# Kernel optimization log

Hardware: AMD Instinct MI355X
Metric: run time of the kernel (lower is better)

Reference implementation:

```python
import jax, jax.numpy as jnp
import numpy as np
import math

H = 8  # num_heads

def setup_inputs() -> dict:
    key = jax.random.key(0)
    ks = jax.random.split(key, 12)
    B, N, M, k = 2, 8192, 8192, 32
    dq, dk, dv = 256, 256, 256
    s = 1.0 / math.sqrt(dq)
    inp = {
        'Q': jax.random.normal(ks[0], (B, N, dq), dtype=jnp.float32),
        'K': jax.random.normal(ks[1], (B, M, dk), dtype=jnp.float32),
        'neighbours': jax.random.randint(ks[2], (B, N, k), 0, M),
        'Wq': jax.random.normal(ks[3], (dq, dv), dtype=jnp.float32) * s,
        'bq': jnp.zeros((dv,), dtype=jnp.float32),
        'Wk': jax.random.normal(ks[4], (dk, dv), dtype=jnp.float32) * s,
        'bk': jnp.zeros((dv,), dtype=jnp.float32),
        'Wv': jax.random.normal(ks[5], (dk, dv), dtype=jnp.float32) * s,
        'bv': jnp.zeros((dv,), dtype=jnp.float32),
        'Wo': jax.random.normal(ks[6], (dv, dv), dtype=jnp.float32) * (1.0 / math.sqrt(dv)),
        'bo': jnp.zeros((dv,), dtype=jnp.float32),
    }
    return inp

def reference(Q, K, neighbours, Wq, bq, Wk, bk, Wv, bv, Wo, bo):
    B, N, _ = Q.shape
    dv = Wq.shape[1]
    ds = dv // H
    # project and split heads (contiguous channel chunks == reshape)
    Qh = (Q @ Wq + bq).reshape(B, N, H, ds)            # [B,N,H,ds]
    Kh = (K @ Wk + bk).reshape(B, -1, H, ds)           # [B,M,H,ds]
    Vh = (K @ Wv + bv).reshape(B, -1, H, ds)           # [B,M,H,ds]
    # gather per-node kNN neighbour keys/values: [B,N,k,H,ds]
    gather = jax.vmap(lambda x, idx: x[idx])
    Kn = gather(Kh, neighbours)
    Vn = gather(Vh, neighbours)
    # scale uses full latent size (faithful to original), not head dim
    scale = 1.0 / math.sqrt(dv)
    E = jnp.einsum('bnhd,bnkhd->bnhk', Qh, Kn) * scale  # [B,N,H,k]
    A = jax.nn.softmax(E, axis=-1)
    AV = jnp.einsum('bnhk,bnkhd->bnhd', A, Vn).reshape(B, N, dv)
    return AV @ Wo + bo
```

## Files before the change

kernel.cpp:

```cpp
#include <hip/hip_runtime.h>
#include <hip/hip_bf16.h>
#include <stdint.h>

typedef unsigned short u16;
typedef __attribute__((ext_vector_type(8))) short short8;
typedef __attribute__((ext_vector_type(4))) float f32x4;

__device__ __forceinline__ u16 f2bf(float f) {
    union { float f; unsigned int i; } v; v.f = f;
    unsigned int b = v.i;
    return (u16)((b + 0x7FFFu + ((b >> 16) & 1u)) >> 16);
}

__device__ __forceinline__ short8 cvt8(float4 a, float4 b) {
    union { __hip_bfloat162 h[4]; short8 s; } u;
    u.h[0] = __float22bfloat162_rn(make_float2(a.x, a.y));
    u.h[1] = __float22bfloat162_rn(make_float2(a.z, a.w));
    u.h[2] = __float22bfloat162_rn(make_float2(b.x, b.y));
    u.h[3] = __float22bfloat162_rn(make_float2(b.z, b.w));
    return u.s;
}

typedef const __attribute__((address_space(1))) void* as1cv;
typedef __attribute__((address_space(3))) void* as3v;
__device__ __forceinline__ void gload16(const void* g, void* l) {
    __builtin_amdgcn_global_load_lds((as1cv)g, (as3v)l, 16, 0, 0);
}

__global__ __launch_bounds__(256) void wprep(
    const float* __restrict__ W0, const float* __restrict__ W1,
    const float* __restrict__ W2, const float* __restrict__ W3,
    u16* __restrict__ T0, u16* __restrict__ T1,
    u16* __restrict__ T2, u16* __restrict__ T3)
{
    const float* W = blockIdx.z == 0 ? W0 : blockIdx.z == 1 ? W1 : blockIdx.z == 2 ? W2 : W3;
    u16*        T  = blockIdx.z == 0 ? T0 : blockIdx.z == 1 ? T1 : blockIdx.z == 2 ? T2 : T3;
    __shared__ u16 ts[64][65];
    int k0 = blockIdx.x * 64, n0 = blockIdx.y * 64;
    int t = threadIdx.x;
    int r = t >> 2, cq = (t & 3) * 16;
    const float4* src = reinterpret_cast<const float4*>(W + (k0 + r) * 256 + n0 + cq);
    for (int u = 0; u < 4; ++u) {
        float4 v = src[u];
        int c = cq + u * 4;
        ts[r][c + 0] = f2bf(v.x); ts[r][c + 1] = f2bf(v.y);
        ts[r][c + 2] = f2bf(v.z); ts[r][c + 3] = f2bf(v.w);
    }
    __syncthreads();
    u16* dst = T + (n0 + r) * 256 + k0 + cq;
    for (int u = 0; u < 16; ++u) dst[u] = ts[cq + u][r];
}

__global__ __launch_bounds__(256) void gemm_proj(
    const float* __restrict__ Q, const float* __restrict__ K,
    const u16* __restrict__ Wtq, const u16* __restrict__ Wtk, const u16* __restrict__ Wtv,
    const float* __restrict__ bq, const float* __restrict__ bk, const float* __restrict__ bv,
    u16* __restrict__ Qh, u16* __restrict__ Kh, u16* __restrict__ Vh)
{
    int z = blockIdx.z;
    const float* Af   = (z == 0) ? Q   : K;
    const u16*   Wt   = (z == 0) ? Wtq : (z == 1) ? Wtk : Wtv;
    const float* bias = (z == 0) ? bq  : (z == 1) ? bk  : bv;
    u16*         C    = (z == 0) ? Qh  : (z == 1) ? Kh  : Vh;

    __shared__ float Asf[128 * 64];
    __shared__ u16   Bs[128 * 64];

    int t = threadIdx.x;
    int lane = t & 63, w = t >> 6;
    int row0 = blockIdx.x * 128, col0 = blockIdx.y * 128;
    int wr = (w >> 1) * 64, wc = (w & 1) * 64;
    int qd = lane >> 4, md = lane & 15;

    f32x4 acc[4][4] = {};

    for (int kt = 0; kt < 256; kt += 64) {
#pragma unroll
        for (int u = 0; u < 8; ++u) {
            int chunk = w * 8 + u;
            int s = chunk * 64 + lane;
            int r = s >> 4, c = s & 15;
            gload16(Af + (size_t)(row0 + r) * 256 + kt + ((c ^ (r & 15)) * 4),
                    (char*)Asf + chunk * 1024);
        }
#pragma unroll
        for (int u = 0; u < 4; ++u) {
            int chunk = w * 4 + u;
            int s = chunk * 64 + lane;
            int r = s >> 3, c = s & 7;
            gload16(Wt + (size_t)(col0 + r) * 256 + kt + ((c ^ (r & 7)) * 8),
                    (char*)Bs + chunk * 1024);
        }
        __syncthreads();
#pragma unroll
        for (int ks = 0; ks < 64; ks += 32) {
            short8 af[4], bf[4];
#pragma unroll
            for (int i = 0; i < 4; ++i) {
                int ar = wr + i * 16 + md;
                int c0 = (ks >> 2) + qd * 2;
                int x = ar & 15;
                float4 fa0 = reinterpret_cast<const float4*>(Asf)[ar * 16 + (c0 ^ x)];
                float4 fa1 = reinterpret_cast<const float4*>(Asf)[ar * 16 + ((c0 + 1) ^ x)];
                af[i] = cvt8(fa0, fa1);
            }
#pragma unroll
            for (int j = 0; j < 4; ++j) {
                int br = wc + j * 16 + md;
                int slot = ((ks >> 3) + qd) ^ (br & 7);
                bf[j] = reinterpret_cast<const short8*>(Bs)[br * 8 + slot];
            }
#pragma unroll
            for (int i = 0; i < 4; ++i)
#pragma unroll
                for (int j = 0; j < 4; ++j)
                    acc[i][j] = __builtin_amdgcn_mfma_f32_16x16x32_bf16(
                        af[i], bf[j], acc[i][j], 0, 0, 0);
        }
        __syncthreads();
    }

#pragma unroll
    for (int i = 0; i < 4; ++i)
#pragma unroll
        for (int j = 0; j < 4; ++j) {
            int col = col0 + wc + j * 16 + md;
            float b = bias[col];
#pragma unroll
            for (int r = 0; r < 4; ++r) {
                int row = row0 + wr + i * 16 + qd * 4 + r;
                C[(size_t)row * 256 + col] = f2bf(acc[i][j][r] + b);
            }
        }
}

__global__ __launch_bounds__(256) void gemm_out(
    const u16* __restrict__ Ab, const u16* __restrict__ Wt,
    const float* __restrict__ bias, float* __restrict__ Cout)
{
    __shared__ u16 As[64 * 64];
    __shared__ u16 Bs[128 * 64];

    int t = threadIdx.x;
    int lane = t & 63, w = t >> 6;
    int row0 = blockIdx.x * 64, col0 = blockIdx.y * 128;
    int wr = (w >> 1) * 32, wc = (w & 1) * 64;
    int qd = lane >> 4, md = lane & 15;

    f32x4 acc[2][4] = {};

    for (int kt = 0; kt < 256; kt += 64) {
#pragma unroll
        for (int u = 0; u < 2; ++u) {
            int chunk = w * 2 + u;
            int s = chunk * 64 + lane;
            int r = s >> 3, c = s & 7;
            gload16(Ab + (size_t)(row0 + r) * 256 + kt + ((c ^ (r & 7)) * 8),
                    (char*)As + chunk * 1024);
        }
#pragma unroll
        for (int u = 0; u < 4; ++u) {
            int chunk = w * 4 + u;
            int s = chunk * 64 + lane;
            int r = s >> 3, c = s & 7;
            gload16(Wt + (size_t)(col0 + r) * 256 + kt + ((c ^ (r & 7)) * 8),
                    (char*)Bs + chunk * 1024);
        }
        __syncthreads();
#pragma unroll
        for (int ks = 0; ks < 64; ks += 32) {
            short8 af[2], bf[4];
#pragma unroll
            for (int i = 0; i < 2; ++i) {
                int ar = wr + i * 16 + md;
                int slot = ((ks >> 3) + qd) ^ (ar & 7);
                af[i] = reinterpret_cast<const short8*>(As)[ar * 8 + slot];
            }
#pragma unroll
            for (int j = 0; j < 4; ++j) {
                int br = wc + j * 16 + md;
                int slot = ((ks >> 3) + qd) ^ (br & 7);
                bf[j] = reinterpret_cast<const short8*>(Bs)[br * 8 + slot];
            }
#pragma unroll
            for (int i = 0; i < 2; ++i)
#pragma unroll
                for (int j = 0; j < 4; ++j)
                    acc[i][j] = __builtin_amdgcn_mfma_f32_16x16x32_bf16(
                        af[i], bf[j], acc[i][j], 0, 0, 0);
        }
        __syncthreads();
    }

#pragma unroll
    for (int i = 0; i < 2; ++i)
#pragma unroll
        for (int j = 0; j < 4; ++j) {
            int col = col0 + wc + j * 16 + md;
            float b = bias[col];
#pragma unroll
            for (int r = 0; r < 4; ++r) {
                int row = row0 + wr + i * 16 + qd * 4 + r;
                Cout[(size_t)row * 256 + col] = acc[i][j][r] + b;
            }
        }
}

__global__ __launch_bounds__(256) void attn(
    const u16* __restrict__ Qh, const u16* __restrict__ Kh, const u16* __restrict__ Vh,
    const int* __restrict__ nbr, u16* __restrict__ AVb)
{
    __shared__ float qs[4][256];
    __shared__ float as_[4][256];
    __shared__ int jb[4][32];

    int t = threadIdx.x;
    int row0 = blockIdx.x * 4;
    int b = row0 >> 13;

#pragma unroll
    for (int rr = 0; rr < 2; ++rr) {
        int idx = rr * 256 + t;
        int r = idx >> 7, c = (idx & 127) * 2;
        unsigned int v = *reinterpret_cast<const unsigned int*>(
            Qh + (size_t)(row0 + r) * 256 + c);
        union { unsigned int i; float f; } lo, hi;
        lo.i = v << 16; hi.i = v & 0xffff0000u;
        qs[r][c] = lo.f; qs[r][c + 1] = hi.f;
    }
    if (t < 128) {
        int r = t >> 5, j = t & 31;
        int ji = nbr[(size_t)(row0 + r) * 32 + j];
        jb[r][j] = ((b << 13) + ji) << 9;
    }
    __syncthreads();

    int h = t >> 5, j = t & 31;
#pragma unroll
    for (int r = 0; r < 4; ++r) {
        const char* kp = (const char*)Kh + jb[r][j] + h * 64;
        uint4 kw[4];
        kw[0] = *reinterpret_cast<const uint4*>(kp);
        kw[1] = *reinterpret_cast<const uint4*>(kp + 16);
        kw[2] = *reinterpret_cast<const uint4*>(kp + 32);
        kw[3] = *reinterpret_cast<const uint4*>(kp + 48);
        const float* q = &qs[r][h * 32];
        float e = 0.f;
#pragma unroll
        for (int cq4 = 0; cq4 < 4; ++cq4) {
            unsigned int wds[4] = {kw[cq4].x, kw[cq4].y, kw[cq4].z, kw[cq4].w};
#pragma unroll
            for (int u = 0; u < 4; ++u) {
                union { unsigned int i; float f; } lo, hi;
                lo.i = wds[u] << 16; hi.i = wds[u] & 0xffff0000u;
                e += q[cq4 * 8 + u * 2] * lo.f + q[cq4 * 8 + u * 2 + 1] * hi.f;
            }
        }
        e *= 0.0625f;
        float m = e;
        for (int off = 16; off; off >>= 1) m = fmaxf(m, __shfl_xor(m, off, 32));
        float p = __expf(e - m);
        float s = p;
        for (int off = 16; off; off >>= 1) s += __shfl_xor(s, off, 32);
        as_[r][t] = p / s;
    }
    __syncthreads();

    {
        int r = t >> 6, c2 = t & 63;
        int hh = c2 >> 3;
        float wv[32];
#pragma unroll
        for (int u = 0; u < 8; ++u)
            *reinterpret_cast<float4*>(&wv[u * 4]) =
                *reinterpret_cast<const float4*>(&as_[r][hh * 32 + u * 4]);
        float a0 = 0.f, a1 = 0.f, a2 = 0.f, a3 = 0.f;
#pragma unroll
        for (int jj = 0; jj < 32; ++jj) {
            int off = __builtin_amdgcn_readfirstlane(jb[r][jj]);
            uint2 v = *reinterpret_cast<const uint2*>(
                (const char*)Vh + off + c2 * 8);
            union { unsigned int i; float f; } l0, h0, l1, h1;
            l0.i = v.x << 16; h0.i = v.x & 0xffff0000u;
            l1.i = v.y << 16; h1.i = v.y & 0xffff0000u;
            float wgt = wv[jj];
            a0 += wgt * l0.f; a1 += wgt * h0.f;
            a2 += wgt * l1.f; a3 += wgt * h1.f;
        }
        u16 o[4] = {f2bf(a0), f2bf(a1), f2bf(a2), f2bf(a3)};
        *reinterpret_cast<uint2*>(AVb + (size_t)(row0 + r) * 256 + c2 * 4) =
            *reinterpret_cast<const uint2*>(o);
    }
}

extern "C" void kernel_launch(void* const* d_in, const int* in_sizes, int n_in,
                              void* d_out, int out_size, void* d_ws, size_t ws_size,
                              hipStream_t stream) {
    const float* Q   = (const float*)d_in[0];
    const float* K   = (const float*)d_in[1];
    const int*   nbr = (const int*)d_in[2];
    const float* Wq  = (const float*)d_in[3];
    const float* bq  = (const float*)d_in[4];
    const float* Wk  = (const float*)d_in[5];
    const float* bk  = (const float*)d_in[6];
    const float* Wv  = (const float*)d_in[7];
    const float* bv  = (const float*)d_in[8];
    const float* Wo  = (const float*)d_in[9];
    const float* bo  = (const float*)d_in[10];
    float* out = (float*)d_out;

    char* ws = (char*)d_ws;
    size_t off = 0;
    auto alloc = [&](size_t bytes) -> void* {
        void* p = ws + off;
        off += (bytes + 255) & ~(size_t)255;
        return p;
    };
    const size_t MN = 16384;
    u16* Wtq = (u16*)alloc(256 * 256 * 2);
    u16* Wtk = (u16*)alloc(256 * 256 * 2);
    u16* Wtv = (u16*)alloc(256 * 256 * 2);
    u16* Wto = (u16*)alloc(256 * 256 * 2);
    u16* Qh  = (u16*)alloc(MN * 256 * 2);
    u16* Kh  = (u16*)alloc(MN * 256 * 2);
    u16* Vh  = (u16*)alloc(MN * 256 * 2);
    u16* AVb = (u16*)alloc(MN * 256 * 2);

    wprep<<<dim3(4, 4, 4), 256, 0, stream>>>(Wq, Wk, Wv, Wo, Wtq, Wtk, Wtv, Wto);
    gemm_proj<<<dim3(128, 2, 3), 256, 0, stream>>>(Q, K, Wtq, Wtk, Wtv,
                                                   bq, bk, bv, Qh, Kh, Vh);
    attn<<<dim3(4096), 256, 0, stream>>>(Qh, Kh, Vh, nbr, AVb);
    gemm_out<<<dim3(256, 2), 256, 0, stream>>>(AVb, Wto, bo, out);
}
```

Measured before the change: 171.0 us.

## Restructure kNN attention kernel to one wave per row with register softmax

The attention kernel now assigns one 64-lane wave per query row. Each half-wave handles 16 neighbours, and each lane covers 8 contiguous channels loaded as 16-byte vectors. Q stays in registers, the scores are reduced with lane shuffles, and the softmax is computed in registers before the V accumulation. This removes the shared-memory staging of Q and the attention weights and one of the block barriers, and it widens the V loads. In exchange it adds more shuffles and register pressure, and it drops the explicit __syncthreads after jbs is written. That is safe only because each wave reads only its own jbs row, which relies on wave-synchronous execution.

```diff
diff --git a/kernel.cpp b/kernel.cpp
--- a/kernel.cpp
+++ b/kernel.cpp
@@ -25,6 +25,12 @@
 typedef __attribute__((address_space(3))) void* as3v;
 __device__ __forceinline__ void gload16(const void* g, void* l) {
     __builtin_amdgcn_global_load_lds((as1cv)g, (as3v)l, 16, 0, 0);
+}
+
+__device__ __forceinline__ void up2(unsigned int v, float& lo, float& hi) {
+    union { unsigned int i; float f; } a, b;
+    a.i = v << 16; b.i = v & 0xffff0000u;
+    lo = a.f; hi = b.f;
 }
 
 __global__ __launch_bounds__(256) void wprep(
@@ -210,86 +216,79 @@
     const u16* __restrict__ Qh, const u16* __restrict__ Kh, const u16* __restrict__ Vh,
     const int* __restrict__ nbr, u16* __restrict__ AVb)
 {
-    __shared__ float qs[4][256];
-    __shared__ float as_[4][256];
-    __shared__ int jb[4][32];
+    __shared__ int jbs[4][32];
 
     int t = threadIdx.x;
-    int row0 = blockIdx.x * 4;
-    int b = row0 >> 13;
-
-#pragma unroll
-    for (int rr = 0; rr < 2; ++rr) {
-        int idx = rr * 256 + t;
-        int r = idx >> 7, c = (idx & 127) * 2;
-        unsigned int v = *reinterpret_cast<const unsigned int*>(
-            Qh + (size_t)(row0 + r) * 256 + c);
-        union { unsigned int i; float f; } lo, hi;
-        lo.i = v << 16; hi.i = v & 0xffff0000u;
-        qs[r][c] = lo.f; qs[r][c + 1] = hi.f;
-    }
-    if (t < 128) {
-        int r = t >> 5, j = t & 31;
-        int ji = nbr[(size_t)(row0 + r) * 32 + j];
-        jb[r][j] = ((b << 13) + ji) << 9;
-    }
-    __syncthreads();
-
-    int h = t >> 5, j = t & 31;
-#pragma unroll
-    for (int r = 0; r < 4; ++r) {
-        const char* kp = (const char*)Kh + jb[r][j] + h * 64;
-        uint4 kw[4];
-        kw[0] = *reinterpret_cast<const uint4*>(kp);
-        kw[1] = *reinterpret_cast<const uint4*>(kp + 16);
-        kw[2] = *reinterpret_cast<const uint4*>(kp + 32);
-        kw[3] = *reinterpret_cast<const uint4*>(kp + 48);
-        const float* q = &qs[r][h * 32];
-        float e = 0.f;
-#pragma unroll
-        for (int cq4 = 0; cq4 < 4; ++cq4) {
-            unsigned int wds[4] = {kw[cq4].x, kw[cq4].y, kw[cq4].z, kw[cq4].w};
-#pragma unroll
-            for (int u = 0; u < 4; ++u) {
-                union { unsigned int i; float f; } lo, hi;
-                lo.i = wds[u] << 16; hi.i = wds[u] & 0xffff0000u;
-                e += q[cq4 * 8 + u * 2] * lo.f + q[cq4 * 8 + u * 2 + 1] * hi.f;
-            }
-        }
-        e *= 0.0625f;
-        float m = e;
-        for (int off = 16; off; off >>= 1) m = fmaxf(m, __shfl_xor(m, off, 32));
-        float p = __expf(e - m);
-        float s = p;
-        for (int off = 16; off; off >>= 1) s += __shfl_xor(s, off, 32);
-        as_[r][t] = p / s;
-    }
-    __syncthreads();
-
+    int w = t >> 6, lane = t & 63;
+    int row = blockIdx.x * 4 + w;
+    int b = row >> 13;
+    int bbase = b << 13;
+
+    int c8 = lane & 31;
+    int jh = lane >> 5;
+
+    if (lane < 32) {
+        int ji = nbr[(size_t)row * 32 + lane];
+        jbs[w][lane] = (bbase + ji) * 256;
+    }
+
+    float qf[8];
     {
-        int r = t >> 6, c2 = t & 63;
-        int hh = c2 >> 3;
-        float wv[32];
-#pragma unroll
-        for (int u = 0; u < 8; ++u)
-            *reinterpret_cast<float4*>(&wv[u * 4]) =
-                *reinterpret_cast<const float4*>(&as_[r][hh * 32 + u * 4]);
-        float a0 = 0.f, a1 = 0.f, a2 = 0.f, a3 = 0.f;
-#pragma unroll
-        for (int jj = 0; jj < 32; ++jj) {
-            int off = __builtin_amdgcn_readfirstlane(jb[r][jj]);
-            uint2 v = *reinterpret_cast<const uint2*>(
-                (const char*)Vh + off + c2 * 8);
-            union { unsigned int i; float f; } l0, h0, l1, h1;
-            l0.i = v.x << 16; h0.i = v.x & 0xffff0000u;
-            l1.i = v.y << 16; h1.i = v.y & 0xffff0000u;
-            float wgt = wv[jj];
-            a0 += wgt * l0.f; a1 += wgt * h0.f;
-            a2 += wgt * l1.f; a3 += wgt * h1.f;
-        }
-        u16 o[4] = {f2bf(a0), f2bf(a1), f2bf(a2), f2bf(a3)};
-        *reinterpret_cast<uint2*>(AVb + (size_t)(row0 + r) * 256 + c2 * 4) =
-            *reinterpret_cast<const uint2*>(o);
+        uint4 qw = *reinterpret_cast<const uint4*>(Qh + (size_t)row * 256 + c8 * 8);
+        up2(qw.x, qf[0], qf[1]); up2(qw.y, qf[2], qf[3]);
+        up2(qw.z, qf[4], qf[5]); up2(qw.w, qf[6], qf[7]);
+    }
+
+    float e16[16];
+#pragma unroll
+    for (int jj = 0; jj < 16; ++jj) {
+        int koff = jbs[w][jh * 16 + jj];
+        uint4 kw = *reinterpret_cast<const uint4*>(Kh + (size_t)koff + c8 * 8);
+        float k0, k1;
+        float p = 0.f;
+        up2(kw.x, k0, k1); p = fmaf(qf[0], k0, p); p = fmaf(qf[1], k1, p);
+        up2(kw.y, k0, k1); p = fmaf(qf[2], k0, p); p = fmaf(qf[3], k1, p);
+        up2(kw.z, k0, k1); p = fmaf(qf[4], k0, p); p = fmaf(qf[5], k1, p);
+        up2(kw.w, k0, k1); p = fmaf(qf[6], k0, p); p = fmaf(qf[7], k1, p);
+        p += __shfl_xor(p, 1);
+        p += __shfl_xor(p, 2);
+        e16[jj] = p * 0.0625f;
+    }
+
+    float m = e16[0];
+#pragma unroll
+    for (int jj = 1; jj < 16; ++jj) m = fmaxf(m, e16[jj]);
+    m = fmaxf(m, __shfl_xor(m, 32));
+    float s = 0.f;
+#pragma unroll
+    for (int jj = 0; jj < 16; ++jj) { e16[jj] = __expf(e16[jj] - m); s += e16[jj]; }
+    s += __shfl_xor(s, 32);
+    float rs = 1.0f / s;
+#pragma unroll
+    for (int jj = 0; jj < 16; ++jj) e16[jj] *= rs;
+
+    float acc[8] = {};
+#pragma unroll
+    for (int jj = 0; jj < 16; ++jj) {
+        int voff = jbs[w][jh * 16 + jj];
+        uint4 vv = *reinterpret_cast<const uint4*>(Vh + (size_t)voff + c8 * 8);
+        float v0, v1;
+        float wgt = e16[jj];
+        up2(vv.x, v0, v1); acc[0] = fmaf(wgt, v0, acc[0]); acc[1] = fmaf(wgt, v1, acc[1]);
+        up2(vv.y, v0, v1); acc[2] = fmaf(wgt, v0, acc[2]); acc[3] = fmaf(wgt, v1, acc[3]);
+        up2(vv.z, v0, v1); acc[4] = fmaf(wgt, v0, acc[4]); acc[5] = fmaf(wgt, v1, acc[5]);
+        up2(vv.w, v0, v1); acc[6] = fmaf(wgt, v0, acc[6]); acc[7] = fmaf(wgt, v1, acc[7]);
+    }
+#pragma unroll
+    for (int u = 0; u < 8; ++u) acc[u] += __shfl_xor(acc[u], 32);
+
+    if (lane < 32) {
+        union { __hip_bfloat162 h[4]; uint4 u4; } o;
+        o.h[0] = __float22bfloat162_rn(make_float2(acc[0], acc[1]));
+        o.h[1] = __float22bfloat162_rn(make_float2(acc[2], acc[3]));
+        o.h[2] = __float22bfloat162_rn(make_float2(acc[4], acc[5]));
+        o.h[3] = __float22bfloat162_rn(make_float2(acc[6], acc[7]));
+        *reinterpret_cast<uint4*>(AVb + (size_t)row * 256 + c8 * 8) = o.u4;
     }
 }
 
```

Result: faster. 161.5 us (-5.6%).
